# Optimization experiments

Measured on AMD Instinct MI355X. Metric: run time of the kernel, lower is better.

The kernel has to match this reference:

```python
import jax, jax.numpy as jnp
import numpy as np

H, W, WS, NUM_HEADS = 64, 64, 1, 8
N = H * W
K_NEI = (2 * WS + 1) ** 2  # 9 neighbors incl. center

# Precompute static neighbor index table + validity mask (same order as the
# torch double loop over i, j offsets).
_rows = np.arange(N) // W
_cols = np.arange(N) % W
_offs = [(i, j) for i in range(-WS, WS + 1) for j in range(-WS, WS + 1)]
_r = _rows[:, None] + np.array([o[0] for o in _offs])[None, :]
_c = _cols[:, None] + np.array([o[1] for o in _offs])[None, :]
_valid = (_r >= 0) & (_r < H) & (_c >= 0) & (_c < W)
NEI_IDX = jnp.asarray(np.where(_valid, _r * W + _c, 0), dtype=jnp.int32)   # [N, 9]
NEI_MASK = jnp.asarray(_valid)                                             # [N, 9]


def setup_inputs() -> dict:
    key = jax.random.key(0)
    ks = jax.random.split(key, 6)
    B, D = 2, 256
    return {
        "x1": jax.random.normal(ks[0], (B, N, D), dtype=jnp.float32),
        "x2": jax.random.normal(ks[1], (B, N, D), dtype=jnp.float32),
        "Wq": jax.random.normal(ks[2], (D, D), dtype=jnp.float32) * 0.02,
        "Wk": jax.random.normal(ks[3], (D, D), dtype=jnp.float32) * 0.02,
        "Wv": jax.random.normal(ks[4], (D, D), dtype=jnp.float32) * 0.02,
        "Wo": jax.random.normal(ks[5], (D, D), dtype=jnp.float32) * 0.02,
        "bq": jnp.zeros((D,), jnp.float32),
        "bk": jnp.zeros((D,), jnp.float32),
        "bv": jnp.zeros((D,), jnp.float32),
        "bo": jnp.zeros((D,), jnp.float32),
    }


def neighborhood_fuse(x2):
    # x2: [B, N, D] -> x2_fused: [B, N, D]
    B, N_, D = x2.shape
    nei = x2[:, NEI_IDX, :]                                    # [B, N, 9, D]
    center = x2                                                # [B, N, D]
    # combined = [center] ++ neighbors (center is duplicated, as in the source)
    combined = jnp.concatenate([center[:, :, None, :], nei], axis=2)  # [B, N, 10, D]
    mask = jnp.concatenate(
        [jnp.ones((N_, 1), dtype=bool), NEI_MASK], axis=1)     # [N, 10]
    scores = jnp.einsum("bnd,bnkd->bnk", center, combined) / jnp.sqrt(
        jnp.asarray(D, x2.dtype))
    scores = jnp.where(mask[None], scores, jnp.finfo(scores.dtype).min)
    w = jax.nn.softmax(scores, axis=-1)                        # [B, N, 10]
    return jnp.einsum("bnk,bnkd->bnd", w, combined)


def mha(q_in, k_in, v_in, Wq, bq, Wk, bk, Wv, bv, Wo, bo):
    B, Nq, D = q_in.shape
    h, hd = NUM_HEADS, D // NUM_HEADS
    q = (q_in @ Wq.T + bq).reshape(B, Nq, h, hd)
    k = (k_in @ Wk.T + bk).reshape(B, -1, h, hd)
    v = (v_in @ Wv.T + bv).reshape(B, -1, h, hd)
    scores = jnp.einsum("bqhd,bkhd->bhqk", q, k) / jnp.sqrt(
        jnp.asarray(hd, q.dtype))
    attn = jax.nn.softmax(scores, axis=-1)
    out = jnp.einsum("bhqk,bkhd->bqhd", attn, v).reshape(B, Nq, D)
    return out @ Wo.T + bo


def reference(x1, x2, Wq, Wk, Wv, Wo, bq, bk, bv, bo):
    x2_fused = neighborhood_fuse(x2)
    return mha(x1, x2_fused, x2_fused, Wq, bq, Wk, bk, Wv, bv, Wo, bo)
```

## Files before the change

### kernel.cpp

```cpp
#include <hip/hip_runtime.h>
#include <hip/hip_bf16.h>
#include <math.h>

#define NPOS 4096
#define DMODEL 256
#define NHEADS 8
#define HDIM 32
#define BATCH 2

typedef __bf16 bf16x8 __attribute__((ext_vector_type(8)));
typedef __bf16 bf16x4 __attribute__((ext_vector_type(4)));
typedef float  f32x4  __attribute__((ext_vector_type(4)));

__global__ __launch_bounds__(256) void fuse_kernel(const float* __restrict__ x2,
                                                   float* __restrict__ x2f) {
  int wave = threadIdx.x >> 6;
  int lane = threadIdx.x & 63;
  int p = (blockIdx.x << 2) + wave;
  int b = p >> 12;
  int n = p & 4095;
  int row = n >> 6, col = n & 63;
  const float4* xb = (const float4*)(x2 + (size_t)b * NPOS * DMODEL);
  float4 c4 = xb[(size_t)n * 64 + lane];
  float4 nb[9];
  float sc[10];
  {
    float part = c4.x * c4.x + c4.y * c4.y + c4.z * c4.z + c4.w * c4.w;
    #pragma unroll
    for (int off = 1; off < 64; off <<= 1) part += __shfl_xor(part, off);
    sc[0] = part * 0.0625f;
  }
  #pragma unroll
  for (int k = 0; k < 9; k++) {
    int di = k / 3 - 1, dj = k % 3 - 1;
    int r = row + di, c = col + dj;
    bool valid = (r >= 0) && (r < 64) && (c >= 0) && (c < 64);
    int nn = valid ? (r * 64 + c) : 0;
    nb[k] = xb[(size_t)nn * 64 + lane];
    float pp = c4.x * nb[k].x + c4.y * nb[k].y + c4.z * nb[k].z + c4.w * nb[k].w;
    #pragma unroll
    for (int off = 1; off < 64; off <<= 1) pp += __shfl_xor(pp, off);
    sc[k + 1] = valid ? pp * 0.0625f : -3.0e38f;
  }
  float m = sc[0];
  #pragma unroll
  for (int k = 1; k < 10; k++) m = fmaxf(m, sc[k]);
  float w[10], wsum = 0.f;
  #pragma unroll
  for (int k = 0; k < 10; k++) { w[k] = expf(sc[k] - m); wsum += w[k]; }
  float inv = 1.0f / wsum;
  float4 o;
  o.x = c4.x * w[0]; o.y = c4.y * w[0]; o.z = c4.z * w[0]; o.w = c4.w * w[0];
  #pragma unroll
  for (int k = 0; k < 9; k++) {
    o.x += nb[k].x * w[k + 1];
    o.y += nb[k].y * w[k + 1];
    o.z += nb[k].z * w[k + 1];
    o.w += nb[k].w * w[k + 1];
  }
  o.x *= inv; o.y *= inv; o.z *= inv; o.w *= inv;
  ((float4*)(x2f + (size_t)b * NPOS * DMODEL))[(size_t)n * 64 + lane] = o;
}

template <int MODE>
__global__ __launch_bounds__(256) void proj_gemm(const float* __restrict__ A,
                                                 const float* __restrict__ Wt,
                                                 const float* __restrict__ bias,
                                                 void* __restrict__ Cout) {
  __shared__ float As_t[32][68];
  __shared__ float Ws_t[32][68];
  int m0 = blockIdx.x * 64;
  int j0 = blockIdx.y * 64;
  int t = threadIdx.x;
  int tx = t & 15, ty = t >> 4;
  float acc[4][4] = {};
  for (int k0 = 0; k0 < 256; k0 += 32) {
    __syncthreads();
    {
      int r = t >> 3;
      int c4 = (t & 7) * 4;
      float4 a0 = *(const float4*)&A[(size_t)(m0 + r) * 256 + k0 + c4];
      float4 a1 = *(const float4*)&A[(size_t)(m0 + r + 32) * 256 + k0 + c4];
      float4 w0 = *(const float4*)&Wt[(size_t)(j0 + r) * 256 + k0 + c4];
      float4 w1 = *(const float4*)&Wt[(size_t)(j0 + r + 32) * 256 + k0 + c4];
      As_t[c4 + 0][r] = a0.x; As_t[c4 + 1][r] = a0.y; As_t[c4 + 2][r] = a0.z; As_t[c4 + 3][r] = a0.w;
      As_t[c4 + 0][r + 32] = a1.x; As_t[c4 + 1][r + 32] = a1.y; As_t[c4 + 2][r + 32] = a1.z; As_t[c4 + 3][r + 32] = a1.w;
      Ws_t[c4 + 0][r] = w0.x; Ws_t[c4 + 1][r] = w0.y; Ws_t[c4 + 2][r] = w0.z; Ws_t[c4 + 3][r] = w0.w;
      Ws_t[c4 + 0][r + 32] = w1.x; Ws_t[c4 + 1][r + 32] = w1.y; Ws_t[c4 + 2][r + 32] = w1.z; Ws_t[c4 + 3][r + 32] = w1.w;
    }
    __syncthreads();
    #pragma unroll
    for (int kk = 0; kk < 32; kk++) {
      float4 a4 = *(const float4*)&As_t[kk][ty * 4];
      float4 b4 = *(const float4*)&Ws_t[kk][tx * 4];
      acc[0][0] += a4.x * b4.x; acc[0][1] += a4.x * b4.y; acc[0][2] += a4.x * b4.z; acc[0][3] += a4.x * b4.w;
      acc[1][0] += a4.y * b4.x; acc[1][1] += a4.y * b4.y; acc[1][2] += a4.y * b4.z; acc[1][3] += a4.y * b4.w;
      acc[2][0] += a4.z * b4.x; acc[2][1] += a4.z * b4.y; acc[2][2] += a4.z * b4.z; acc[2][3] += a4.z * b4.w;
      acc[3][0] += a4.w * b4.x; acc[3][1] += a4.w * b4.y; acc[3][2] += a4.w * b4.z; acc[3][3] += a4.w * b4.w;
    }
  }
  if (MODE == 0) {
    float* C = (float*)Cout;
    #pragma unroll
    for (int i = 0; i < 4; i++) {
      int m = m0 + ty * 4 + i;
      #pragma unroll
      for (int j = 0; j < 4; j++) {
        int jj = j0 + tx * 4 + j;
        C[(size_t)m * 256 + jj] = acc[i][j] + bias[jj];
      }
    }
  } else if (MODE == 1) {
    unsigned short* C = (unsigned short*)Cout;
    int jj0 = j0 + tx * 4;
    int head = jj0 >> 5, dd0 = jj0 & 31;
    #pragma unroll
    for (int i = 0; i < 4; i++) {
      int m = m0 + ty * 4 + i;
      int b = m >> 12, n = m & 4095;
      bf16x4 pk;
      #pragma unroll
      for (int j = 0; j < 4; j++) pk[j] = (__bf16)(acc[i][j] + bias[jj0 + j]);
      *(bf16x4*)(C + (((size_t)(b * NHEADS + head) * NPOS + n) * HDIM + dd0)) = pk;
    }
  } else {
    unsigned short* C = (unsigned short*)Cout;
    int m00 = m0 + ty * 4;
    int b = m00 >> 12, n0 = m00 & 4095;
    #pragma unroll
    for (int j = 0; j < 4; j++) {
      int jj = j0 + tx * 4 + j;
      int head = jj >> 5, dd = jj & 31;
      bf16x4 pk;
      #pragma unroll
      for (int i = 0; i < 4; i++) pk[i] = (__bf16)(acc[i][j] + bias[jj]);
      *(bf16x4*)(C + (((size_t)(b * NHEADS + head) * HDIM + dd) * NPOS + n0)) = pk;
    }
  }
}

__global__ __launch_bounds__(256, 2) void attn_mfma(const unsigned short* __restrict__ Qg,
                                                    const unsigned short* __restrict__ Kg,
                                                    const unsigned short* __restrict__ VTg,
                                                    float* __restrict__ O) {
  __shared__ unsigned short Pl[4][2][2048];
  int bid = blockIdx.x;
  int lid = (bid & 7) * 64 + (bid >> 3);
  int bh = lid >> 5;
  int qblk = (lid & 31) * 128;
  int w = threadIdx.x >> 6;
  int lane = threadIdx.x & 63;
  int q4 = lane & 15, g = lane >> 4;
  int qbase = qblk + w * 32;
  const unsigned short* Qb  = Qg  + (size_t)bh * NPOS * HDIM;
  const unsigned short* Kb  = Kg  + (size_t)bh * NPOS * HDIM;
  const unsigned short* VTb = VTg + (size_t)bh * HDIM * NPOS;

  bf16x8 qf[2];
  qf[0] = *(const bf16x8*)(Qb + (size_t)(qbase + q4) * HDIM + g * 8);
  qf[1] = *(const bf16x8*)(Qb + (size_t)(qbase + 16 + q4) * HDIM + g * 8);

  f32x4 os[2][2] = {};
  float m2[2] = {-1e30f, -1e30f};
  float lsum[2] = {0.f, 0.f};
  const int swz = (q4 & 7) << 3;
  const float c = 0.17677669529663687f;

  for (int kt = 0; kt < 64; kt++) {
    unsigned short* Pw = Pl[w][kt & 1];
    const unsigned short* Kt = Kb + (size_t)kt * 64 * HDIM;
    bf16x8 kf[4];
    #pragma unroll
    for (int mf = 0; mf < 4; mf++)
      kf[mf] = *(const bf16x8*)(Kt + (size_t)(mf * 16 + q4) * HDIM + g * 8);
    bf16x8 vf[2][2];
    #pragma unroll
    for (int dm = 0; dm < 2; dm++)
      #pragma unroll
      for (int kk = 0; kk < 2; kk++)
        vf[dm][kk] = *(const bf16x8*)(VTb + (size_t)(dm * 16 + q4) * NPOS + kt * 64 + kk * 32 + g * 8);

    f32x4 s[4][2];
    #pragma unroll
    for (int mf = 0; mf < 4; mf++)
      #pragma unroll
      for (int nf = 0; nf < 2; nf++) {
        f32x4 z = {0.f, 0.f, 0.f, 0.f};
        s[mf][nf] = __builtin_amdgcn_mfma_f32_16x16x32_bf16(kf[mf], qf[nf], z, 0, 0, 0);
      }

    float tm[2];
    #pragma unroll
    for (int nf = 0; nf < 2; nf++) {
      float a = fmaxf(fmaxf(s[0][nf][0], s[0][nf][1]), fmaxf(s[0][nf][2], s[0][nf][3]));
      #pragma unroll
      for (int mf = 1; mf < 4; mf++) {
        float b2 = fmaxf(fmaxf(s[mf][nf][0], s[mf][nf][1]), fmaxf(s[mf][nf][2], s[mf][nf][3]));
        a = fmaxf(a, b2);
      }
      a = fmaxf(a, __shfl_xor(a, 16));
      a = fmaxf(a, __shfl_xor(a, 32));
      tm[nf] = a * c;
    }
    float n0 = fmaxf(m2[0], tm[0]), n1 = fmaxf(m2[1], tm[1]);
    if (__any((n0 > m2[0] + 8.f) || (n1 > m2[1] + 8.f))) {
      float r0 = __expf(m2[0] - n0), r1 = __expf(m2[1] - n1);
      lsum[0] *= r0; lsum[1] *= r1;
      os[0][0] *= r0; os[1][0] *= r0;
      os[0][1] *= r1; os[1][1] *= r1;
      m2[0] = n0; m2[1] = n1;
    }

    #pragma unroll
    for (int nf = 0; nf < 2; nf++) {
      float mm = m2[nf];
      #pragma unroll
      for (int mf = 0; mf < 4; mf++) {
        bf16x4 pk;
        #pragma unroll
        for (int r = 0; r < 4; r++) {
          float p = __expf(s[mf][nf][r] * c - mm);
          lsum[nf] += p;
          pk[r] = (__bf16)p;
        }
        int k0 = (mf * 16 + g * 4) ^ swz;
        *(bf16x4*)(Pw + (nf * 16 + q4) * 64 + k0) = pk;
      }
    }
    asm volatile("s_waitcnt lgkmcnt(0)" ::: "memory");
    __builtin_amdgcn_sched_barrier(0);

    #pragma unroll
    for (int nf = 0; nf < 2; nf++) {
      bf16x8 pb[2];
      #pragma unroll
      for (int kk = 0; kk < 2; kk++) {
        int k0 = (kk * 32 + g * 8) ^ swz;
        pb[kk] = *(const bf16x8*)(Pw + (nf * 16 + q4) * 64 + k0);
      }
      #pragma unroll
      for (int dm = 0; dm < 2; dm++)
        #pragma unroll
        for (int kk = 0; kk < 2; kk++)
          os[dm][nf] = __builtin_amdgcn_mfma_f32_16x16x32_bf16(vf[dm][kk], pb[kk], os[dm][nf], 0, 0, 0);
    }
  }

  #pragma unroll
  for (int nf = 0; nf < 2; nf++) {
    lsum[nf] += __shfl_xor(lsum[nf], 16);
    lsum[nf] += __shfl_xor(lsum[nf], 32);
  }
  float inv[2] = {1.f / lsum[0], 1.f / lsum[1]};
  int b = bh >> 3, head = bh & 7;
  #pragma unroll
  for (int nf = 0; nf < 2; nf++) {
    int q = qbase + nf * 16 + q4;
    float* Orow = O + ((size_t)(b * NPOS + q)) * DMODEL + head * HDIM;
    #pragma unroll
    for (int dm = 0; dm < 2; dm++) {
      f32x4 v = os[dm][nf] * inv[nf];
      *(f32x4*)(Orow + dm * 16 + g * 4) = v;
    }
  }
}

extern "C" void kernel_launch(void* const* d_in, const int* in_sizes, int n_in,
                              void* d_out, int out_size, void* d_ws, size_t ws_size,
                              hipStream_t stream) {
  const float* x1 = (const float*)d_in[0];
  const float* x2 = (const float*)d_in[1];
  const float* Wq = (const float*)d_in[2];
  const float* Wk = (const float*)d_in[3];
  const float* Wv = (const float*)d_in[4];
  const float* Wo = (const float*)d_in[5];
  const float* bq = (const float*)d_in[6];
  const float* bk = (const float*)d_in[7];
  const float* bv = (const float*)d_in[8];
  const float* bo = (const float*)d_in[9];

  float* ws = (float*)d_ws;
  const size_t S = (size_t)BATCH * NPOS * DMODEL;
  float* x2f  = ws;
  float* attn = ws + S;
  unsigned short* ub = (unsigned short*)(ws + 2 * S);
  unsigned short* Qb  = ub;
  unsigned short* Kb  = ub + S;
  unsigned short* VTb = ub + 2 * S;
  float* out = (float*)d_out;

  fuse_kernel<<<2048, 256, 0, stream>>>(x2, x2f);

  dim3 pg(128, 4);
  proj_gemm<1><<<pg, 256, 0, stream>>>(x1,  Wq, bq, (void*)Qb);
  proj_gemm<1><<<pg, 256, 0, stream>>>(x2f, Wk, bk, (void*)Kb);
  proj_gemm<2><<<pg, 256, 0, stream>>>(x2f, Wv, bv, (void*)VTb);

  attn_mfma<<<512, 256, 0, stream>>>(Qb, Kb, VTb, attn);

  proj_gemm<0><<<pg, 256, 0, stream>>>(attn, Wo, bo, (void*)out);
}
```

Measured before the change: 268.1 us.

## Keep softmax probabilities in registers instead of LDS round-trip in attention

The attention kernel no longer writes the exp'd score tile to shared memory and reads it back in the B-operand layout. It reuses the QK^T MFMA output registers directly as the PV operand and permutes the key ordering to match. V^T is now loaded as two 4-element halves per fragment so its k-index order lines up with the register layout of P. This removes LDS stores, loads and the waitcnt barrier per key tile, at the cost of smaller 8-byte global loads for V.

```diff
diff --git a/kernel.cpp b/kernel.cpp
--- a/kernel.cpp
+++ b/kernel.cpp
@@ -143,7 +143,6 @@
                                                     const unsigned short* __restrict__ Kg,
                                                     const unsigned short* __restrict__ VTg,
                                                     float* __restrict__ O) {
-  __shared__ unsigned short Pl[4][2][2048];
   int bid = blockIdx.x;
   int lid = (bid & 7) * 64 + (bid >> 3);
   int bh = lid >> 5;
@@ -163,22 +162,27 @@
   f32x4 os[2][2] = {};
   float m2[2] = {-1e30f, -1e30f};
   float lsum[2] = {0.f, 0.f};
-  const int swz = (q4 & 7) << 3;
   const float c = 0.17677669529663687f;
 
   for (int kt = 0; kt < 64; kt++) {
-    unsigned short* Pw = Pl[w][kt & 1];
     const unsigned short* Kt = Kb + (size_t)kt * 64 * HDIM;
     bf16x8 kf[4];
     #pragma unroll
     for (int mf = 0; mf < 4; mf++)
       kf[mf] = *(const bf16x8*)(Kt + (size_t)(mf * 16 + q4) * HDIM + g * 8);
+
     bf16x8 vf[2][2];
     #pragma unroll
-    for (int dm = 0; dm < 2; dm++)
-      #pragma unroll
-      for (int kk = 0; kk < 2; kk++)
-        vf[dm][kk] = *(const bf16x8*)(VTb + (size_t)(dm * 16 + q4) * NPOS + kt * 64 + kk * 32 + g * 8);
+    for (int dm = 0; dm < 2; dm++) {
+      const unsigned short* Vrow = VTb + (size_t)(dm * 16 + q4) * NPOS + kt * 64;
+      #pragma unroll
+      for (int kk = 0; kk < 2; kk++) {
+        bf16x4 vlo = *(const bf16x4*)(Vrow + kk * 32 + g * 4);
+        bf16x4 vhi = *(const bf16x4*)(Vrow + kk * 32 + 16 + g * 4);
+        #pragma unroll
+        for (int r = 0; r < 4; r++) { vf[dm][kk][r] = vlo[r]; vf[dm][kk][4 + r] = vhi[r]; }
+      }
+    }
 
     f32x4 s[4][2];
     #pragma unroll
@@ -216,33 +220,29 @@
       float mm = m2[nf];
       #pragma unroll
       for (int mf = 0; mf < 4; mf++) {
-        bf16x4 pk;
         #pragma unroll
         for (int r = 0; r < 4; r++) {
           float p = __expf(s[mf][nf][r] * c - mm);
           lsum[nf] += p;
-          pk[r] = (__bf16)p;
+          s[mf][nf][r] = p;
         }
-        int k0 = (mf * 16 + g * 4) ^ swz;
-        *(bf16x4*)(Pw + (nf * 16 + q4) * 64 + k0) = pk;
-      }
-    }
-    asm volatile("s_waitcnt lgkmcnt(0)" ::: "memory");
-    __builtin_amdgcn_sched_barrier(0);
+      }
+    }
 
     #pragma unroll
     for (int nf = 0; nf < 2; nf++) {
-      bf16x8 pb[2];
       #pragma unroll
       for (int kk = 0; kk < 2; kk++) {
-        int k0 = (kk * 32 + g * 8) ^ swz;
-        pb[kk] = *(const bf16x8*)(Pw + (nf * 16 + q4) * 64 + k0);
-      }
-      #pragma unroll
-      for (int dm = 0; dm < 2; dm++)
+        bf16x8 pb;
         #pragma unroll
-        for (int kk = 0; kk < 2; kk++)
-          os[dm][nf] = __builtin_amdgcn_mfma_f32_16x16x32_bf16(vf[dm][kk], pb[kk], os[dm][nf], 0, 0, 0);
+        for (int r = 0; r < 4; r++) {
+          pb[r]     = (__bf16)s[2 * kk][nf][r];
+          pb[4 + r] = (__bf16)s[2 * kk + 1][nf][r];
+        }
+        #pragma unroll
+        for (int dm = 0; dm < 2; dm++)
+          os[dm][nf] = __builtin_amdgcn_mfma_f32_16x16x32_bf16(vf[dm][kk], pb, os[dm][nf], 0, 0, 0);
+      }
     }
   }
 
```

Result: slower. 317.1 us (+18.3%).
